# Kernel optimization log

Measured on AMD Instinct MI355X. Metric: run time of the kernel, lower is better.

## Reference

```python
import jax, jax.numpy as jnp
import numpy as np

B, L, D = 4, 2048, 1024
H, KD, VD = 16, 64, 64
EPS = 1e-5


def setup_inputs() -> dict:
    key = jax.random.key(0)
    ks = jax.random.split(key, 12)
    s_in = 1.0 / np.sqrt(D)
    s_out = 1.0 / np.sqrt(H * VD)
    return {
        "queries": jax.random.normal(ks[0], (B, L, D), dtype=jnp.float32),
        "Wq": jax.random.uniform(ks[1], (D, H * KD), jnp.float32, -s_in, s_in),
        "bq": jax.random.uniform(ks[2], (H * KD,), jnp.float32, -s_in, s_in),
        "Wk": jax.random.uniform(ks[3], (D, H * KD), jnp.float32, -s_in, s_in),
        "bk": jax.random.uniform(ks[4], (H * KD,), jnp.float32, -s_in, s_in),
        "Wv": jax.random.uniform(ks[5], (D, H * VD), jnp.float32, -s_in, s_in),
        "bv": jax.random.uniform(ks[6], (H * VD,), jnp.float32, -s_in, s_in),
        "Wo": jax.random.uniform(ks[7], (H * VD, D), jnp.float32, -s_out, s_out),
        "bo": jax.random.uniform(ks[8], (D,), jnp.float32, -s_out, s_out),
        "gamma": jnp.ones((D,), jnp.float32),
        "beta": jnp.zeros((D,), jnp.float32),
    }


def reference(queries, Wq, bq, Wk, bk, Wv, bv, Wo, bo, gamma, beta):
    # QKV projections -> [B, L, H, head_dim]
    q = (queries @ Wq + bq).reshape(B, L, H, KD)
    k = (queries @ Wk + bk).reshape(B, L, H, KD)
    v = (queries @ Wv + bv).reshape(B, L, H, VD)
    # scaled dot-product attention per head: scores [B, H, Lq, Lk]
    scores = jnp.einsum("bqhd,bkhd->bhqk", q, k) / np.sqrt(KD).astype(np.float32)
    attn = jax.nn.softmax(scores, axis=-1)
    out = jnp.einsum("bhqk,bkhd->bqhd", attn, v).reshape(B, L, H * VD)
    # out projection (dropout is identity in eval), residual + LayerNorm
    res = out @ Wo + bo + queries
    mu = jnp.mean(res, axis=-1, keepdims=True)
    var = jnp.var(res, axis=-1, keepdims=True)
    return (res - mu) / jnp.sqrt(var + EPS) * gamma + beta
```

## Files before the change

kernel.cpp:

```cpp
#include <hip/hip_runtime.h>
#include <hip/hip_bf16.h>

#define BATCH 4
#define SEQ   2048
#define DIM   1024
#define NHEAD 16
#define HDIM  64
#define EPS_LN 1e-5f
#define QSCALE 0.18033688011112042f

typedef __attribute__((ext_vector_type(8))) short short8;
typedef __attribute__((ext_vector_type(4))) float f32x4;
typedef __attribute__((ext_vector_type(4))) unsigned uint32x4;

__device__ __forceinline__ unsigned short f2bf(float x) {
    __hip_bfloat16 h = __float2bfloat16(x);
    return *reinterpret_cast<unsigned short*>(&h);
}
__device__ __forceinline__ unsigned int pack2bf(float a, float b) {
    __hip_bfloat162 h = __float22bfloat162_rn(float2{a, b});
    return *reinterpret_cast<unsigned int*>(&h);
}

__device__ __forceinline__ void pl32_swap(unsigned& a, unsigned& b) {
    asm("v_permlane32_swap_b32 %0, %1" : "+v"(a), "+v"(b));
}
__device__ __forceinline__ void pl16_swap(unsigned& a, unsigned& b) {
    asm("v_permlane16_swap_b32 %0, %1" : "+v"(a), "+v"(b));
}

__device__ __forceinline__ void gl_lds16(const void* g, void* l) {
    __builtin_amdgcn_global_load_lds(
        (const __attribute__((address_space(1))) unsigned int*)g,
        (__attribute__((address_space(3))) unsigned int*)l,
        16, 0, 0);
}

__global__ __launch_bounds__(256) void prep_kernel(const float* __restrict__ W0,
                                                   const float* __restrict__ W1,
                                                   const float* __restrict__ W2,
                                                   const float* __restrict__ W3,
                                                   const float* __restrict__ queries,
                                                   unsigned short* __restrict__ Wqkvt,
                                                   unsigned short* __restrict__ Wot,
                                                   unsigned short* __restrict__ qout)
{
    const int z = blockIdx.z;
    const int t = threadIdx.x;

    if (z == 4) {
        const int nthr = 16 * 16 * 256;
        int i = (blockIdx.y * 16 + blockIdx.x) * 256 + t;
        for (int it = 0; it < (BATCH * SEQ * DIM / 4) / nthr; it++, i += nthr) {
            float4 v = ((const float4*)queries)[i];
            ushort4 u;
            u.x = f2bf(v.x); u.y = f2bf(v.y); u.z = f2bf(v.z); u.w = f2bf(v.w);
            ((ushort4*)qout)[i] = u;
        }
        return;
    }

    __shared__ float Ts[64][65];
    const float* W = (z == 0) ? W0 : (z == 1) ? W1 : (z == 2) ? W2 : W3;
    unsigned short* Wt = (z == 3) ? Wot : (Wqkvt + (size_t)z * DIM * DIM);

    const int k0 = blockIdx.y * 64, n0 = blockIdx.x * 64;
    const int lr = t >> 2, lq = t & 3;

#pragma unroll
    for (int i = 0; i < 4; i++) {
        float4 v = *(const float4*)(W + (size_t)(k0 + lr) * DIM + n0 + (lq * 4 + i) * 4);
        Ts[lr][(lq * 4 + i) * 4 + 0] = v.x;
        Ts[lr][(lq * 4 + i) * 4 + 1] = v.y;
        Ts[lr][(lq * 4 + i) * 4 + 2] = v.z;
        Ts[lr][(lq * 4 + i) * 4 + 3] = v.w;
    }
    __syncthreads();
#pragma unroll
    for (int i = 0; i < 4; i++) {
        const int c = lq * 16 + i * 4;
        ushort4 u;
        u.x = f2bf(Ts[c + 0][lr]);
        u.y = f2bf(Ts[c + 1][lr]);
        u.z = f2bf(Ts[c + 2][lr]);
        u.w = f2bf(Ts[c + 3][lr]);
        *(ushort4*)(Wt + (size_t)(n0 + lr) * DIM + k0 + c) = u;
    }
}

__global__ __launch_bounds__(256) void gemm_qkv(const unsigned short* __restrict__ A,
                                                const unsigned short* __restrict__ Bt,
                                                const float* __restrict__ bq,
                                                const float* __restrict__ bk,
                                                const float* __restrict__ bv,
                                                unsigned short* __restrict__ Qbf,
                                                unsigned short* __restrict__ Kbf,
                                                unsigned short* __restrict__ Vtb)
{
    __shared__ __attribute__((aligned(16))) unsigned short As[128 * 32];
    __shared__ __attribute__((aligned(16))) unsigned short Bs[128 * 32];

    const int tid = threadIdx.x;
    const int w = tid >> 6, lane = tid & 63;
    const int col = lane & 15, quad = lane >> 4;
    const int wm = (w >> 1) * 64, wn = (w & 1) * 64;
    const int m0 = blockIdx.y * 128, n0 = blockIdx.x * 128;

    f32x4 acc[4][4] = {};
    const int srow = tid >> 2, sc4 = tid & 3;

    for (int k0 = 0; k0 < DIM; k0 += 32) {
        __syncthreads();
#pragma unroll
        for (int it = 0; it < 2; it++) {
            gl_lds16(A  + (size_t)(m0 + srow + it * 64) * DIM + k0 + sc4 * 8,
                     (char*)As + w * 1024 + it * 4096);
            gl_lds16(Bt + (size_t)(n0 + srow + it * 64) * DIM + k0 + sc4 * 8,
                     (char*)Bs + w * 1024 + it * 4096);
        }
        __syncthreads();

        short8 af[4], bf[4];
#pragma unroll
        for (int mt = 0; mt < 4; mt++) af[mt] = *(short8*)&As[(wm + mt * 16 + col) * 32 + quad * 8];
#pragma unroll
        for (int nt = 0; nt < 4; nt++) bf[nt] = *(short8*)&Bs[(wn + nt * 16 + col) * 32 + quad * 8];

#pragma unroll
        for (int mt = 0; mt < 4; mt++)
#pragma unroll
            for (int nt = 0; nt < 4; nt++)
                acc[mt][nt] = __builtin_amdgcn_mfma_f32_16x16x32_bf16(af[mt], bf[nt], acc[mt][nt], 0, 0, 0);
    }

    const int sector = n0 >> 10;
    const float* bias = (sector == 0) ? bq : (sector == 1) ? bk : bv;

#pragma unroll
    for (int nt = 0; nt < 4; nt++) {
        const int n = n0 + wn + nt * 16 + col;
        const int nloc = n - (sector << 10);
        const float bvv = bias[nloc];
#pragma unroll
        for (int mt = 0; mt < 4; mt++) {
            const int mbase = m0 + wm + mt * 16 + quad * 4;
            if (sector == 0) {
#pragma unroll
                for (int r = 0; r < 4; r++)
                    Qbf[(size_t)(mbase + r) * DIM + nloc] = f2bf((acc[mt][nt][r] + bvv) * QSCALE);
            } else if (sector == 1) {
#pragma unroll
                for (int r = 0; r < 4; r++)
                    Kbf[(size_t)(mbase + r) * DIM + nloc] = f2bf(acc[mt][nt][r] + bvv);
            } else {
                const int h = nloc >> 6, d = nloc & 63;
                const int b = mbase >> 11, l = mbase & 2047;
                ushort4 u;
                u.x = f2bf(acc[mt][nt][0] + bvv);
                u.y = f2bf(acc[mt][nt][1] + bvv);
                u.z = f2bf(acc[mt][nt][2] + bvv);
                u.w = f2bf(acc[mt][nt][3] + bvv);
                *(ushort4*)(Vtb + ((size_t)((b * NHEAD + h) * HDIM + d)) * SEQ + l) = u;
            }
        }
    }
}

__global__ __launch_bounds__(256) void gemm_out(const unsigned short* __restrict__ A,
                                                const unsigned short* __restrict__ Bt,
                                                const float* __restrict__ bias,
                                                const float* __restrict__ resid,
                                                float* __restrict__ Cout)
{
    __shared__ __attribute__((aligned(16))) unsigned short As[128 * 32];
    __shared__ __attribute__((aligned(16))) unsigned short Bs[128 * 32];

    const int tid = threadIdx.x;
    const int w = tid >> 6, lane = tid & 63;
    const int col = lane & 15, quad = lane >> 4;
    const int wm = (w >> 1) * 64, wn = (w & 1) * 64;
    const int m0 = blockIdx.y * 128, n0 = blockIdx.x * 128;

    f32x4 acc[4][4] = {};
    const int srow = tid >> 2, sc4 = tid & 3;

    for (int k0 = 0; k0 < DIM; k0 += 32) {
        __syncthreads();
#pragma unroll
        for (int it = 0; it < 2; it++) {
            gl_lds16(A  + (size_t)(m0 + srow + it * 64) * DIM + k0 + sc4 * 8,
                     (char*)As + w * 1024 + it * 4096);
            gl_lds16(Bt + (size_t)(n0 + srow + it * 64) * DIM + k0 + sc4 * 8,
                     (char*)Bs + w * 1024 + it * 4096);
        }
        __syncthreads();

        short8 af[4], bf[4];
#pragma unroll
        for (int mt = 0; mt < 4; mt++) af[mt] = *(short8*)&As[(wm + mt * 16 + col) * 32 + quad * 8];
#pragma unroll
        for (int nt = 0; nt < 4; nt++) bf[nt] = *(short8*)&Bs[(wn + nt * 16 + col) * 32 + quad * 8];

#pragma unroll
        for (int mt = 0; mt < 4; mt++)
#pragma unroll
            for (int nt = 0; nt < 4; nt++)
                acc[mt][nt] = __builtin_amdgcn_mfma_f32_16x16x32_bf16(af[mt], bf[nt], acc[mt][nt], 0, 0, 0);
    }

#pragma unroll
    for (int nt = 0; nt < 4; nt++) {
        const int n = n0 + wn + nt * 16 + col;
        const float bvv = bias[n];
#pragma unroll
        for (int mt = 0; mt < 4; mt++) {
            const int mbase = m0 + wm + mt * 16 + quad * 4;
#pragma unroll
            for (int r = 0; r < 4; r++) {
                const size_t off = (size_t)(mbase + r) * DIM + n;
                Cout[off] = acc[mt][nt][r] + bvv + resid[off];
            }
        }
    }
}

#define KP 72
__global__ __launch_bounds__(256) void attn_mfma(const unsigned short* __restrict__ Qb,
                                                 const unsigned short* __restrict__ Kb,
                                                 const unsigned short* __restrict__ Vt,
                                                 unsigned short* __restrict__ Ob)
{
    __shared__ __attribute__((aligned(16))) unsigned short Ks[64 * KP];
    __shared__ __attribute__((aligned(16))) unsigned short Vs[64 * KP];

    const int tid = threadIdx.x;
    const int w = tid >> 6, lane = tid & 63;
    const int col = lane & 15, quad = lane >> 4;

    const int bh  = blockIdx.x & 63;
    const int qt_ = blockIdx.x >> 6;
    const int b   = bh >> 4;
    const int h   = bh & 15;

    const int q0 = qt_ * 128 + w * 32;

    short8 qf[2][2];
#pragma unroll
    for (int qt = 0; qt < 2; qt++) {
        const size_t base = ((size_t)(b * SEQ) + q0 + qt * 16 + col) * DIM + h * HDIM + quad * 8;
        qf[qt][0] = *(const short8*)(Qb + base);
        qf[qt][1] = *(const short8*)(Qb + base + 32);
    }

    short8 onesf;
    {
        const short v = (col == 0) ? (short)0x3F80 : (short)0;
        onesf = short8{v, v, v, v, v, v, v, v};
    }

    f32x4 o[4][2] = {};
    f32x4 od[2]   = {};

    const size_t kbase0 = ((size_t)(b * SEQ)) * DIM + h * HDIM;
    const size_t vbase0 = ((size_t)((b * NHEAD + h) * HDIM)) * SEQ;

    const int srow = tid >> 3, sc = tid & 7;

    for (int kt = 0; kt < SEQ / 64; kt++) {
        __syncthreads();
#pragma unroll
        for (int it = 0; it < 2; it++) {
            const int row = srow + it * 32;
            *(int4*)&Ks[row * KP + sc * 8] = *(const int4*)(Kb + kbase0 + (size_t)(kt * 64 + row) * DIM + sc * 8);
            *(int4*)&Vs[row * KP + sc * 8] = *(const int4*)(Vt + vbase0 + (size_t)row * SEQ + kt * 64 + sc * 8);
        }
        __syncthreads();

        short8 pf[2][2];
#pragma unroll
        for (int f = 0; f < 2; f++) {
            short8 kfe0 = *(short8*)&Ks[((f * 2 + 0) * 16 + col) * KP + quad * 8];
            short8 kfe1 = *(short8*)&Ks[((f * 2 + 0) * 16 + col) * KP + quad * 8 + 32];
            short8 kfo0 = *(short8*)&Ks[((f * 2 + 1) * 16 + col) * KP + quad * 8];
            short8 kfo1 = *(short8*)&Ks[((f * 2 + 1) * 16 + col) * KP + quad * 8 + 32];
#pragma unroll
            for (int qt = 0; qt < 2; qt++) {
                f32x4 se = {};
                se = __builtin_amdgcn_mfma_f32_16x16x32_bf16(kfe0, qf[qt][0], se, 0, 0, 0);
                se = __builtin_amdgcn_mfma_f32_16x16x32_bf16(kfe1, qf[qt][1], se, 0, 0, 0);
                f32x4 so = {};
                so = __builtin_amdgcn_mfma_f32_16x16x32_bf16(kfo0, qf[qt][0], so, 0, 0, 0);
                so = __builtin_amdgcn_mfma_f32_16x16x32_bf16(kfo1, qf[qt][1], so, 0, 0, 0);

                unsigned a0 = pack2bf(__builtin_amdgcn_exp2f(se[0]), __builtin_amdgcn_exp2f(se[1]));
                unsigned b0 = pack2bf(__builtin_amdgcn_exp2f(se[2]), __builtin_amdgcn_exp2f(se[3]));
                unsigned a1 = pack2bf(__builtin_amdgcn_exp2f(so[0]), __builtin_amdgcn_exp2f(so[1]));
                unsigned b1 = pack2bf(__builtin_amdgcn_exp2f(so[2]), __builtin_amdgcn_exp2f(so[3]));

                pl32_swap(a0, a1);
                pl32_swap(b0, b1);
                pl16_swap(a0, a1);
                pl16_swap(b0, b1);

                uint32x4 cv = {a0, b0, a1, b1};
                pf[qt][f] = __builtin_bit_cast(short8, cv);
            }
        }

#pragma unroll
        for (int qt = 0; qt < 2; qt++) {
            od[qt] = __builtin_amdgcn_mfma_f32_16x16x32_bf16(onesf, pf[qt][0], od[qt], 0, 0, 0);
            od[qt] = __builtin_amdgcn_mfma_f32_16x16x32_bf16(onesf, pf[qt][1], od[qt], 0, 0, 0);
        }

#pragma unroll
        for (int mt = 0; mt < 4; mt++) {
            short8 vf0 = *(short8*)&Vs[(mt * 16 + col) * KP + quad * 8];
            short8 vf1 = *(short8*)&Vs[(mt * 16 + col) * KP + quad * 8 + 32];
#pragma unroll
            for (int qt = 0; qt < 2; qt++) {
                o[mt][qt] = __builtin_amdgcn_mfma_f32_16x16x32_bf16(vf0, pf[qt][0], o[mt][qt], 0, 0, 0);
                o[mt][qt] = __builtin_amdgcn_mfma_f32_16x16x32_bf16(vf1, pf[qt][1], o[mt][qt], 0, 0, 0);
            }
        }
    }

#pragma unroll
    for (int qt = 0; qt < 2; qt++) {
        const float den = __shfl(od[qt][0], col);
        const float inv = 1.f / den;
        const size_t rowoff = ((size_t)(b * SEQ) + q0 + qt * 16 + col) * DIM + h * HDIM;
#pragma unroll
        for (int mt = 0; mt < 4; mt++) {
            ushort4 u;
            u.x = f2bf(o[mt][qt][0] * inv);
            u.y = f2bf(o[mt][qt][1] * inv);
            u.z = f2bf(o[mt][qt][2] * inv);
            u.w = f2bf(o[mt][qt][3] * inv);
            *(ushort4*)(Ob + rowoff + mt * 16 + quad * 4) = u;
        }
    }
}

__global__ __launch_bounds__(256) void layernorm_kernel(float* __restrict__ res,
                                                        const float* __restrict__ gamma,
                                                        const float* __restrict__ beta)
{
    const int tid = threadIdx.x;
    const int row = blockIdx.x;
    float4 xv = ((const float4*)(res + (size_t)row * DIM))[tid];

    float s  = xv.x + xv.y + xv.z + xv.w;
    float sq = xv.x * xv.x + xv.y * xv.y + xv.z * xv.z + xv.w * xv.w;
#pragma unroll
    for (int off = 32; off; off >>= 1) {
        s  += __shfl_xor(s, off);
        sq += __shfl_xor(sq, off);
    }
    __shared__ float sm[8];
    const int w = tid >> 6, lane = tid & 63;
    if (lane == 0) { sm[w] = s; sm[4 + w] = sq; }
    __syncthreads();
    const float st  = sm[0] + sm[1] + sm[2] + sm[3];
    const float sqt = sm[4] + sm[5] + sm[6] + sm[7];
    const float mu   = st * (1.f / DIM);
    const float var  = sqt * (1.f / DIM) - mu * mu;
    const float rstd = rsqrtf(var + EPS_LN);

    float4 g  = ((const float4*)gamma)[tid];
    float4 be = ((const float4*)beta)[tid];
    float4 o;
    o.x = (xv.x - mu) * rstd * g.x + be.x;
    o.y = (xv.y - mu) * rstd * g.y + be.y;
    o.z = (xv.z - mu) * rstd * g.z + be.z;
    o.w = (xv.w - mu) * rstd * g.w + be.w;
    ((float4*)(res + (size_t)row * DIM))[tid] = o;
}

extern "C" void kernel_launch(void* const* d_in, const int* in_sizes, int n_in,
                              void* d_out, int out_size, void* d_ws, size_t ws_size,
                              hipStream_t stream)
{
    const float* queries = (const float*)d_in[0];
    const float* Wq = (const float*)d_in[1];
    const float* bq = (const float*)d_in[2];
    const float* Wk = (const float*)d_in[3];
    const float* bk = (const float*)d_in[4];
    const float* Wv = (const float*)d_in[5];
    const float* bv = (const float*)d_in[6];
    const float* Wo = (const float*)d_in[7];
    const float* bo = (const float*)d_in[8];
    const float* gamma = (const float*)d_in[9];
    const float* beta  = (const float*)d_in[10];
    float* outp = (float*)d_out;

    const int M = BATCH * SEQ;
    const size_t BUF = (size_t)M * DIM;
    const size_t WSZ = (size_t)DIM * DIM;

    unsigned short* w0  = (unsigned short*)d_ws;
    unsigned short* qin = w0;
    unsigned short* Qbf = w0 + BUF;
    unsigned short* Kbf = w0 + 2 * BUF;
    unsigned short* Vtb = w0 + 3 * BUF;
    unsigned short* Wqkvt = w0 + 4 * BUF;
    unsigned short* Wot   = Wqkvt + 3 * WSZ;
    unsigned short* Obf = qin;

    dim3 blk(256);

    dim3 pgrid(DIM / 64, DIM / 64, 5);
    prep_kernel<<<pgrid, blk, 0, stream>>>(Wq, Wk, Wv, Wo, queries, Wqkvt, Wot, qin);

    dim3 qkvgrid(3 * DIM / 128, M / 128);
    gemm_qkv<<<qkvgrid, blk, 0, stream>>>(qin, Wqkvt, bq, bk, bv, Qbf, Kbf, Vtb);

    attn_mfma<<<BATCH * NHEAD * (SEQ / 128), blk, 0, stream>>>(Qbf, Kbf, Vtb, Obf);

    dim3 ogrid(DIM / 128, M / 128);
    gemm_out<<<ogrid, blk, 0, stream>>>(Obf, Wot, bo, queries, outp);

    layernorm_kernel<<<M, blk, 0, stream>>>(outp, gamma, beta);
}
```

Baseline: 308.9 us.

## Double-buffer K/V tiles in attention with register prefetch and one barrier

Attention K/V shared-memory tiles become double-buffered. The next tile's global loads are issued into registers before the current tile is computed, so memory latency overlaps with the MFMA work. The two barriers per iteration become one explicit waitcnt plus barrier, and s_setprio raises wave priority around the PV MFMA block. This doubles LDS use and adds register pressure for the prefetched int4 values.

```diff
diff --git a/kernel.cpp b/kernel.cpp
--- a/kernel.cpp
+++ b/kernel.cpp
@@ -230,8 +230,8 @@
                                                  const unsigned short* __restrict__ Vt,
                                                  unsigned short* __restrict__ Ob)
 {
-    __shared__ __attribute__((aligned(16))) unsigned short Ks[64 * KP];
-    __shared__ __attribute__((aligned(16))) unsigned short Vs[64 * KP];
+    __shared__ __attribute__((aligned(16))) unsigned short Ks[2][64 * KP];
+    __shared__ __attribute__((aligned(16))) unsigned short Vs[2][64 * KP];
 
     const int tid = threadIdx.x;
     const int w = tid >> 6, lane = tid & 63;
@@ -266,23 +266,41 @@
 
     const int srow = tid >> 3, sc = tid & 7;
 
+    int4 kr[2], vr[2];
+#pragma unroll
+    for (int it = 0; it < 2; it++) {
+        const int row = srow + it * 32;
+        kr[it] = *(const int4*)(Kb + kbase0 + (size_t)row * DIM + sc * 8);
+        vr[it] = *(const int4*)(Vt + vbase0 + (size_t)row * SEQ + sc * 8);
+    }
+
     for (int kt = 0; kt < SEQ / 64; kt++) {
-        __syncthreads();
+        unsigned short* Ksb = Ks[kt & 1];
+        unsigned short* Vsb = Vs[kt & 1];
+
 #pragma unroll
         for (int it = 0; it < 2; it++) {
             const int row = srow + it * 32;
-            *(int4*)&Ks[row * KP + sc * 8] = *(const int4*)(Kb + kbase0 + (size_t)(kt * 64 + row) * DIM + sc * 8);
-            *(int4*)&Vs[row * KP + sc * 8] = *(const int4*)(Vt + vbase0 + (size_t)row * SEQ + kt * 64 + sc * 8);
-        }
-        __syncthreads();
+            *(int4*)&Ksb[row * KP + sc * 8] = kr[it];
+            *(int4*)&Vsb[row * KP + sc * 8] = vr[it];
+        }
+        if (kt + 1 < SEQ / 64) {
+#pragma unroll
+            for (int it = 0; it < 2; it++) {
+                const int row = srow + it * 32;
+                kr[it] = *(const int4*)(Kb + kbase0 + (size_t)((kt + 1) * 64 + row) * DIM + sc * 8);
+                vr[it] = *(const int4*)(Vt + vbase0 + (size_t)row * SEQ + (kt + 1) * 64 + sc * 8);
+            }
+        }
+        asm volatile("s_waitcnt lgkmcnt(0)\n\ts_barrier" ::: "memory");
 
         short8 pf[2][2];
 #pragma unroll
         for (int f = 0; f < 2; f++) {
-            short8 kfe0 = *(short8*)&Ks[((f * 2 + 0) * 16 + col) * KP + quad * 8];
-            short8 kfe1 = *(short8*)&Ks[((f * 2 + 0) * 16 + col) * KP + quad * 8 + 32];
-            short8 kfo0 = *(short8*)&Ks[((f * 2 + 1) * 16 + col) * KP + quad * 8];
-            short8 kfo1 = *(short8*)&Ks[((f * 2 + 1) * 16 + col) * KP + quad * 8 + 32];
+            short8 kfe0 = *(short8*)&Ksb[((f * 2 + 0) * 16 + col) * KP + quad * 8];
+            short8 kfe1 = *(short8*)&Ksb[((f * 2 + 0) * 16 + col) * KP + quad * 8 + 32];
+            short8 kfo0 = *(short8*)&Ksb[((f * 2 + 1) * 16 + col) * KP + quad * 8];
+            short8 kfo1 = *(short8*)&Ksb[((f * 2 + 1) * 16 + col) * KP + quad * 8 + 32];
 #pragma unroll
             for (int qt = 0; qt < 2; qt++) {
                 f32x4 se = {};
@@ -307,6 +325,7 @@
             }
         }
 
+        __builtin_amdgcn_s_setprio(1);
 #pragma unroll
         for (int qt = 0; qt < 2; qt++) {
             od[qt] = __builtin_amdgcn_mfma_f32_16x16x32_bf16(onesf, pf[qt][0], od[qt], 0, 0, 0);
@@ -315,14 +334,15 @@
 
 #pragma unroll
         for (int mt = 0; mt < 4; mt++) {
-            short8 vf0 = *(short8*)&Vs[(mt * 16 + col) * KP + quad * 8];
-            short8 vf1 = *(short8*)&Vs[(mt * 16 + col) * KP + quad * 8 + 32];
+            short8 vf0 = *(short8*)&Vsb[(mt * 16 + col) * KP + quad * 8];
+            short8 vf1 = *(short8*)&Vsb[(mt * 16 + col) * KP + quad * 8 + 32];
 #pragma unroll
             for (int qt = 0; qt < 2; qt++) {
                 o[mt][qt] = __builtin_amdgcn_mfma_f32_16x16x32_bf16(vf0, pf[qt][0], o[mt][qt], 0, 0, 0);
                 o[mt][qt] = __builtin_amdgcn_mfma_f32_16x16x32_bf16(vf1, pf[qt][1], o[mt][qt], 0, 0, 0);
             }
         }
+        __builtin_amdgcn_s_setprio(0);
     }
 
 #pragma unroll
```

Measured after the change: 372.0 us. +20.4%, slower.

## Double-buffer attention K/V tiles with direct global-to-LDS loads and XOR swizzle

Applied to the files above, without the earlier changes.

The attention kernel now loads K and V tiles straight into LDS with gl_lds16 and double-buffers them, so the next tile's fetch overlaps the current tile's MFMA work. The padded LDS layout is replaced by an XOR-swizzled 64-wide layout to avoid bank conflicts. s_setprio raises wave priority around the PV MFMA block, and one barrier per iteration replaces two. LDS use doubles, which may lower occupancy, and correctness depends on the async loads being complete at the barrier.

```diff
diff --git a/kernel.cpp b/kernel.cpp
--- a/kernel.cpp
+++ b/kernel.cpp
@@ -224,18 +224,20 @@
     }
 }
 
-#define KP 72
 __global__ __launch_bounds__(256) void attn_mfma(const unsigned short* __restrict__ Qb,
                                                  const unsigned short* __restrict__ Kb,
                                                  const unsigned short* __restrict__ Vt,
                                                  unsigned short* __restrict__ Ob)
 {
-    __shared__ __attribute__((aligned(16))) unsigned short Ks[64 * KP];
-    __shared__ __attribute__((aligned(16))) unsigned short Vs[64 * KP];
+    __shared__ __attribute__((aligned(16))) unsigned short Ks[2 * 64 * 64];
+    __shared__ __attribute__((aligned(16))) unsigned short Vs[2 * 64 * 64];
 
     const int tid = threadIdx.x;
     const int w = tid >> 6, lane = tid & 63;
     const int col = lane & 15, quad = lane >> 4;
+    const int cs  = col & 7;
+    const int ca  = quad ^ cs;
+    const int cb  = (quad ^ 4) ^ cs;
 
     const int bh  = blockIdx.x & 63;
     const int qt_ = blockIdx.x >> 6;
@@ -264,25 +266,42 @@
     const size_t kbase0 = ((size_t)(b * SEQ)) * DIM + h * HDIM;
     const size_t vbase0 = ((size_t)((b * NHEAD + h) * HDIM)) * SEQ;
 
-    const int srow = tid >> 3, sc = tid & 7;
+    const int lr  = lane >> 3;
+    const int swc = (lane & 7) ^ lr;
+
+#pragma unroll
+    for (int i = 0; i < 2; i++) {
+        const int row = w * 16 + i * 8 + lr;
+        gl_lds16(Kb + kbase0 + (size_t)row * DIM + swc * 8,
+                 (char*)Ks + w * 2048 + i * 1024);
+        gl_lds16(Vt + vbase0 + (size_t)row * SEQ + swc * 8,
+                 (char*)Vs + w * 2048 + i * 1024);
+    }
+    __syncthreads();
 
     for (int kt = 0; kt < SEQ / 64; kt++) {
-        __syncthreads();
-#pragma unroll
-        for (int it = 0; it < 2; it++) {
-            const int row = srow + it * 32;
-            *(int4*)&Ks[row * KP + sc * 8] = *(const int4*)(Kb + kbase0 + (size_t)(kt * 64 + row) * DIM + sc * 8);
-            *(int4*)&Vs[row * KP + sc * 8] = *(const int4*)(Vt + vbase0 + (size_t)row * SEQ + kt * 64 + sc * 8);
-        }
-        __syncthreads();
+        const int cur = kt & 1, nxt = cur ^ 1;
+        const unsigned short* Ksb = Ks + cur * 4096;
+        const unsigned short* Vsb = Vs + cur * 4096;
+
+        if (kt + 1 < SEQ / 64) {
+#pragma unroll
+            for (int i = 0; i < 2; i++) {
+                const int row = w * 16 + i * 8 + lr;
+                gl_lds16(Kb + kbase0 + (size_t)((kt + 1) * 64 + row) * DIM + swc * 8,
+                         (char*)Ks + nxt * 8192 + w * 2048 + i * 1024);
+                gl_lds16(Vt + vbase0 + (size_t)row * SEQ + (kt + 1) * 64 + swc * 8,
+                         (char*)Vs + nxt * 8192 + w * 2048 + i * 1024);
+            }
+        }
 
         short8 pf[2][2];
 #pragma unroll
         for (int f = 0; f < 2; f++) {
-            short8 kfe0 = *(short8*)&Ks[((f * 2 + 0) * 16 + col) * KP + quad * 8];
-            short8 kfe1 = *(short8*)&Ks[((f * 2 + 0) * 16 + col) * KP + quad * 8 + 32];
-            short8 kfo0 = *(short8*)&Ks[((f * 2 + 1) * 16 + col) * KP + quad * 8];
-            short8 kfo1 = *(short8*)&Ks[((f * 2 + 1) * 16 + col) * KP + quad * 8 + 32];
+            short8 kfe0 = *(short8*)&Ksb[((f * 2 + 0) * 16 + col) * 64 + ca * 8];
+            short8 kfe1 = *(short8*)&Ksb[((f * 2 + 0) * 16 + col) * 64 + cb * 8];
+            short8 kfo0 = *(short8*)&Ksb[((f * 2 + 1) * 16 + col) * 64 + ca * 8];
+            short8 kfo1 = *(short8*)&Ksb[((f * 2 + 1) * 16 + col) * 64 + cb * 8];
 #pragma unroll
             for (int qt = 0; qt < 2; qt++) {
                 f32x4 se = {};
@@ -307,6 +326,7 @@
             }
         }
 
+        __builtin_amdgcn_s_setprio(1);
 #pragma unroll
         for (int qt = 0; qt < 2; qt++) {
             od[qt] = __builtin_amdgcn_mfma_f32_16x16x32_bf16(onesf, pf[qt][0], od[qt], 0, 0, 0);
@@ -315,14 +335,17 @@
 
 #pragma unroll
         for (int mt = 0; mt < 4; mt++) {
-            short8 vf0 = *(short8*)&Vs[(mt * 16 + col) * KP + quad * 8];
-            short8 vf1 = *(short8*)&Vs[(mt * 16 + col) * KP + quad * 8 + 32];
+            short8 vf0 = *(short8*)&Vsb[(mt * 16 + col) * 64 + ca * 8];
+            short8 vf1 = *(short8*)&Vsb[(mt * 16 + col) * 64 + cb * 8];
 #pragma unroll
             for (int qt = 0; qt < 2; qt++) {
                 o[mt][qt] = __builtin_amdgcn_mfma_f32_16x16x32_bf16(vf0, pf[qt][0], o[mt][qt], 0, 0, 0);
                 o[mt][qt] = __builtin_amdgcn_mfma_f32_16x16x32_bf16(vf1, pf[qt][1], o[mt][qt], 0, 0, 0);
             }
         }
+        __builtin_amdgcn_s_setprio(0);
+
+        __syncthreads();
     }
 
 #pragma unroll
```

Measured after the change: 322.5 us. 4.4% more time.
